# Kernel optimization log

Measured on AMD Instinct MI355X. Metric: run time of the kernel, lower is better.

## Reference

```python
import jax, jax.numpy as jnp
import numpy as np

TOP_K = 6
CAP_FACTOR = 2.0


def setup_inputs() -> dict:
    key = jax.random.key(0)
    ks = jax.random.split(key, 9)
    B, S, D, F, E, SH = 4, 2048, 512, 256, 64, 2
    return {
        "x": jax.random.normal(ks[0], (B, S, D), jnp.float32),
        "router_w": jax.random.normal(ks[1], (E, D), jnp.float32) * 0.02,
        "bias": jnp.zeros((E,), jnp.float32),
        "shared_w_gate": jax.random.normal(ks[2], (SH, F, D), jnp.float32) * 0.02,
        "shared_w_up": jax.random.normal(ks[3], (SH, F, D), jnp.float32) * 0.02,
        "shared_w_down": jax.random.normal(ks[4], (SH, D, F), jnp.float32) * 0.02,
        "w_gate": jax.random.normal(ks[5], (E, F, D), jnp.float32) * 0.02,
        "w_up": jax.random.normal(ks[6], (E, F, D), jnp.float32) * 0.02,
        "w_down": jax.random.normal(ks[7], (E, D, F), jnp.float32) * 0.02,
    }


def reference(x, router_w, bias, shared_w_gate, shared_w_up, shared_w_down, w_gate, w_up, w_down):
    B, S, D = x.shape
    E = router_w.shape[0]
    K = TOP_K
    N = B * S
    C = max(1, int(N * K * CAP_FACTOR / E))  # static per-expert capacity

    # Router logits with balancing bias (loop_idx=0 row).
    router_logits = jnp.einsum('bsd,ed->bse', x, router_w) + bias

    # Shared experts: averaged SwiGLU over SH experts, fully batched.
    hg = jnp.einsum('bsd,efd->bsef', x, shared_w_gate)
    hu = jnp.einsum('bsd,efd->bsef', x, shared_w_up)
    shared_out = jnp.einsum('bsef,edf->bsd', jax.nn.silu(hg) * hu, shared_w_down)
    shared_out = shared_out / shared_w_gate.shape[0]

    # Top-k routing, renormalised gates.
    router_probs = jax.nn.softmax(router_logits, axis=-1)
    topk_p, topk_i = jax.lax.top_k(router_probs, K)  # [B,S,K]
    topk_p = topk_p / (jnp.sum(topk_p, axis=-1, keepdims=True) + 1e-9)

    x_flat = x.reshape(N, D)
    flat_e = topk_i.reshape(-1)            # [N*K] expert ids
    flat_g = topk_p.reshape(-1)            # [N*K] gates
    token_ids = jnp.repeat(jnp.arange(N), K)

    # Stable sort by expert id -> contiguous expert groups.
    order = jnp.argsort(flat_e)            # jax argsort is stable
    se = flat_e[order]
    st = token_ids[order]
    sg = flat_g[order]

    M = se.shape[0]
    pos = jnp.arange(M)
    is_first = jnp.concatenate([jnp.ones((1,), bool), se[1:] != se[:-1]])
    group_starts = jax.lax.cummax(pos * is_first.astype(pos.dtype))
    slot = pos - group_starts              # position within expert group
    valid = slot < C                       # capacity drop
    safe_slot = jnp.where(valid, slot, C)  # overflow -> scratch slot C

    # Static-shape dispatch buffers (E, C+1, ...); slot C is scratch.
    expert_in = jnp.zeros((E, C + 1, D), x.dtype).at[se, safe_slot].set(x_flat[st])
    expert_gate = jnp.zeros((E, C + 1), x.dtype).at[se, safe_slot].set(sg)
    expert_tok = jnp.full((E, C + 1), N, jnp.int32).at[se, safe_slot].set(st.astype(jnp.int32))
    expert_mask = jnp.zeros((E, C + 1), bool).at[se, safe_slot].set(valid)

    expert_in = expert_in[:, :C]
    expert_gate = expert_gate[:, :C]
    expert_tok = expert_tok[:, :C]
    expert_mask = expert_mask[:, :C]

    # Grouped SwiGLU: three batched GEMMs over experts.
    hg = jnp.einsum('ecd,efd->ecf', expert_in, w_gate)
    hu = jnp.einsum('ecd,efd->ecf', expert_in, w_up)
    expert_out = jnp.einsum('ecf,edf->ecd', jax.nn.silu(hg) * hu, w_down)

    # Combine: scatter-add gated outputs back to tokens; row N is a sink.
    fm = expert_mask.reshape(-1)
    dst = jnp.where(fm, expert_tok.reshape(-1), N)
    fg = jnp.where(fm, expert_gate.reshape(-1), jnp.zeros((), x.dtype))
    sparse = jax.ops.segment_sum(fg[:, None] * expert_out.reshape(-1, D), dst, num_segments=N + 1)[:N]

    return shared_out + sparse.reshape(B, S, D)
```

## Files before the change

kernel.cpp:

```cpp
#include <hip/hip_runtime.h>
#include <hip/hip_bf16.h>
#include <math.h>

#define N_TOK 8192
#define D_DIM 512
#define F_DIM 256
#define E_NUM 64
#define SH_NUM 2
#define K_TOP 6
#define CAP   1536
#define M_ENT (N_TOK * K_TOP)
#define NCHUNK (M_ENT / 256)

#define EW_STRIDE 393216
#define E_TOT (E_NUM + SH_NUM)
#define X_BF_BYTES   (8388608ull)
#define WT_BYTES     ((size_t)E_TOT * EW_STRIDE * 2)
#define TOK_ROUTED   (E_NUM * CAP)
#define TOK_TOTAL    (TOK_ROUTED + SH_NUM * N_TOK)
#define EO_BYTES     ((size_t)TOK_TOTAL * D_DIM * 2)
#define RWT_BYTES    131072ull

typedef __attribute__((ext_vector_type(8))) short bf16x8;
typedef __attribute__((ext_vector_type(8))) short short8;
typedef __attribute__((ext_vector_type(4))) float f32x4;

__device__ __forceinline__ ushort f2bf(float f) {
  union { float f; unsigned u; } c; c.f = f;
  return (ushort)((c.u + 0x7FFFu + ((c.u >> 16) & 1u)) >> 16);
}
__device__ __forceinline__ float bf2f(ushort h) {
  union { unsigned u; float f; } c; c.u = ((unsigned)h) << 16;
  return c.f;
}

__global__ void router_topk(const float* __restrict__ x, const float* __restrict__ rw,
                            const float* __restrict__ bias, int* __restrict__ topk_i,
                            float* __restrict__ topk_p) {
  const int wave = threadIdx.x >> 6;
  const int lane = threadIdx.x & 63;
  const int n = blockIdx.x * 4 + wave;
  if (n >= N_TOK) return;

  const float4* xr = (const float4*)(x + (size_t)n * D_DIM);
  const float4* wr = (const float4*)(rw + (size_t)lane * D_DIM);
  float acc = 0.f;
  #pragma unroll 4
  for (int d4 = 0; d4 < D_DIM / 4; ++d4) {
    float4 xv = xr[d4]; float4 wv = wr[d4];
    acc += xv.x * wv.x + xv.y * wv.y + xv.z * wv.z + xv.w * wv.w;
  }
  float logit = acc + bias[lane];

  float m = logit;
  for (int off = 32; off > 0; off >>= 1) m = fmaxf(m, __shfl_xor(m, off));
  float p = expf(logit - m);
  float s = p;
  for (int off = 32; off > 0; off >>= 1) s += __shfl_xor(s, off);
  float prob = p / s;

  float myp = prob;
  float gsum = 0.f;
  float myg = 0.f; int myi = -1;
  for (int k = 0; k < K_TOP; ++k) {
    float bp = myp; int bi = lane;
    for (int off = 32; off > 0; off >>= 1) {
      float op = __shfl_xor(bp, off); int oi = __shfl_xor(bi, off);
      if (op > bp || (op == bp && oi < bi)) { bp = op; bi = oi; }
    }
    gsum += bp;
    if (lane == k) { myg = bp; myi = bi; }
    if (lane == bi) myp = -1.f;
  }
  if (lane < K_TOP) {
    topk_i[n * K_TOP + lane] = myi;
    topk_p[n * K_TOP + lane] = myg / (gsum + 1e-9f);
  }
}

__device__ __forceinline__ void softmax_topk_write(float logit, int n, int lane,
                                                   int* __restrict__ topk_i,
                                                   float* __restrict__ topk_p) {
  float m = logit;
  for (int off = 32; off > 0; off >>= 1) m = fmaxf(m, __shfl_xor(m, off));
  float p = expf(logit - m);
  float s = p;
  for (int off = 32; off > 0; off >>= 1) s += __shfl_xor(s, off);
  float prob = p / s;

  float myp = prob;
  float gsum = 0.f;
  float myg = 0.f; int myi = -1;
  #pragma unroll 1
  for (int k = 0; k < K_TOP; ++k) {
    float bp = myp; int bi = lane;
    for (int off = 32; off > 0; off >>= 1) {
      float op = __shfl_xor(bp, off); int oi = __shfl_xor(bi, off);
      if (op > bp || (op == bp && oi < bi)) { bp = op; bi = oi; }
    }
    gsum += bp;
    if (lane == k) { myg = bp; myi = bi; }
    if (lane == bi) myp = -1.f;
  }
  if (lane < K_TOP) {
    topk_i[n * K_TOP + lane] = myi;
    topk_p[n * K_TOP + lane] = myg / (gsum + 1e-9f);
  }
}

__global__ void __launch_bounds__(256) router_topk2(
    const float* __restrict__ x, const float* __restrict__ rwt,
    const float* __restrict__ bias, int* __restrict__ topk_i,
    float* __restrict__ topk_p) {
  const int wave = threadIdx.x >> 6;
  const int lane = threadIdx.x & 63;
  const int n0 = blockIdx.x * 32 + wave * 8;

  float acc[8];
  #pragma unroll
  for (int t = 0; t < 8; ++t) acc[t] = 0.f;

  const float4* wv4 = (const float4*)rwt;
  #pragma unroll 2
  for (int k4 = 0; k4 < 128; ++k4) {
    float4 w = wv4[k4 * 64 + lane];
    #pragma unroll
    for (int t = 0; t < 8; ++t) {
      float4 xv = *(const float4*)(x + (size_t)(n0 + t) * D_DIM + k4 * 4);
      acc[t] += xv.x * w.x + xv.y * w.y + xv.z * w.z + xv.w * w.w;
    }
  }
  float b = bias[lane];
  #pragma unroll 1
  for (int t = 0; t < 8; ++t)
    softmax_topk_write(acc[t] + b, n0 + t, lane, topk_i, topk_p);
}

__global__ void hist_kernel(const int* __restrict__ topk_i, int* __restrict__ chunk_hist) {
  __shared__ int h[E_NUM];
  const int tid = threadIdx.x;
  if (tid < E_NUM) h[tid] = 0;
  __syncthreads();
  int e = topk_i[blockIdx.x * 256 + tid];
  atomicAdd(&h[e], 1);
  __syncthreads();
  if (tid < E_NUM) chunk_hist[blockIdx.x * E_NUM + tid] = h[tid];
}

__global__ void scan_kernel(const int* __restrict__ chunk_hist, int* __restrict__ chunk_base) {
  const int e = threadIdx.x;
  int run = 0;
  for (int c = 0; c < NCHUNK; ++c) {
    chunk_base[c * E_NUM + e] = run;
    run += chunk_hist[c * E_NUM + e];
  }
}

__global__ void dispatch_kernel(const int* __restrict__ topk_i, const float* __restrict__ topk_p,
                                const int* __restrict__ chunk_base,
                                int* __restrict__ expert_tok, float* __restrict__ expert_gate,
                                int* __restrict__ entry_row) {
  __shared__ int eid[256];
  const int tid = threadIdx.x;
  const int m = blockIdx.x * 256 + tid;
  const int e = topk_i[m];
  eid[tid] = e;
  __syncthreads();
  int rank = 0;
  for (int t = 0; t < tid; ++t) rank += (eid[t] == e);
  int slot = chunk_base[blockIdx.x * E_NUM + e] + rank;
  int row = -1;
  if (slot < CAP) {
    expert_tok[e * CAP + slot] = m / K_TOP;
    expert_gate[e * CAP + slot] = topk_p[m];
    row = e * CAP + slot;
  }
  if (entry_row) entry_row[m] = row;
}


__global__ void convert_x_misc(const float* __restrict__ x, ushort* __restrict__ xb,
                               const float* __restrict__ rw, float* __restrict__ rwt,
                               int* __restrict__ tok_all, float* __restrict__ gate_all) {
  int b = blockIdx.x;
  if (b < 2048) {
    size_t idx = (size_t)b * 256 + threadIdx.x;
    const float4* s4 = (const float4*)(x + idx * 8);
    float4 v0 = s4[0], v1 = s4[1];
    short8 o;
    o[0] = f2bf(v0.x); o[1] = f2bf(v0.y); o[2] = f2bf(v0.z); o[3] = f2bf(v0.w);
    o[4] = f2bf(v1.x); o[5] = f2bf(v1.y); o[6] = f2bf(v1.z); o[7] = f2bf(v1.w);
    *(short8*)(xb + idx * 8) = o;
  } else if (b < 2080) {
    int idx = (b - 2048) * 256 + threadIdx.x;
    int e = idx >> 7, k4 = idx & 127;
    float4 v = *(const float4*)(rw + (size_t)e * D_DIM + k4 * 4);
    *(float4*)(rwt + ((size_t)k4 * 64 + e) * 4) = v;
  } else {
    int i = (b - 2080) * 256 + threadIdx.x;
    tok_all[TOK_ROUTED + i] = i & (N_TOK - 1);
    gate_all[TOK_ROUTED + i] = 0.5f;
  }
}

__global__ void convert_w(const float* __restrict__ wg_, const float* __restrict__ wu_,
                          const float* __restrict__ wd_, const float* __restrict__ swg,
                          const float* __restrict__ swu, const float* __restrict__ swd,
                          ushort* __restrict__ Wt) {
  int e = blockIdx.x / 12;
  int rem = blockIdx.x - e * 12;
  int p = rem >> 2, q = rem & 3;
  const float* src;
  if (p == 0)      src = (e < E_NUM) ? wg_ + (size_t)e * 131072 : swg + (size_t)(e - E_NUM) * 131072;
  else if (p == 1) src = (e < E_NUM) ? wu_ + (size_t)e * 131072 : swu + (size_t)(e - E_NUM) * 131072;
  else             src = (e < E_NUM) ? wd_ + (size_t)e * 131072 : swd + (size_t)(e - E_NUM) * 131072;
  ushort* dst = Wt + (size_t)e * EW_STRIDE + (size_t)p * 131072;
  #pragma unroll
  for (int i = 0; i < 16; ++i) {
    int d = q * 32768 + i * 2048 + threadIdx.x * 8;
    int ci = d >> 13;
    int r  = d & 8191;
    int nt = r >> 9;
    int rr = r & 511;
    int k8 = rr >> 7;
    int n  = nt * 16 + ((rr >> 3) & 15);
    size_t srcidx;
    if (p < 2) {
      srcidx = (size_t)n * 512 + ci * 32 + k8 * 8;
    } else {
      int np = ci >> 3, kc = ci & 7;
      srcidx = (size_t)(np * 256 + n) * 256 + kc * 32 + k8 * 8;
    }
    const float4* s4 = (const float4*)(src + srcidx);
    float4 v0 = s4[0], v1 = s4[1];
    short8 o;
    o[0] = f2bf(v0.x); o[1] = f2bf(v0.y); o[2] = f2bf(v0.z); o[3] = f2bf(v0.w);
    o[4] = f2bf(v1.x); o[5] = f2bf(v1.y); o[6] = f2bf(v1.z); o[7] = f2bf(v1.w);
    *(short8*)(dst + d) = o;
  }
}

template <bool GATHER>
__global__ void __launch_bounds__(512, 1) ffn_mfma(
    const ushort* __restrict__ xb, const ushort* __restrict__ Wt,
    const int* __restrict__ tok_all, const float* __restrict__ gate_all,
    float* __restrict__ out, ushort* __restrict__ expert_out) {
  int e, tbase;
  {
    int xcd = blockIdx.x & 7;
    int j = blockIdx.x >> 3;
    if (j < 96) {
      int ec = j / 12;
      int mt = j - ec * 12;
      e = ec * 8 + xcd;
      tbase = e * CAP + mt * 128;
      if (tok_all[tbase] < 0) return;
    } else {
      int s = xcd * 16 + (j - 96);
      int sh = s & 1, mt = s >> 1;
      e = E_NUM + sh;
      tbase = TOK_ROUTED + sh * N_TOK + mt * 128;
    }
  }
  const ushort* wbase = Wt + (size_t)e * EW_STRIDE;

  __shared__ ushort Act[32768];
  __shared__ int   toks[128];
  __shared__ float gts[128];

  const int tid = threadIdx.x;
  const int lane = tid & 63;
  const int wid = tid >> 6;
  const int wr = wid >> 2;
  const int wc = wid & 3;
  const int rl = lane & 15;
  const int hi = lane >> 4;

  if (tid < 128) {
    int t = tok_all[tbase + tid];
    toks[tid] = t;
    gts[tid] = (t >= 0) ? gate_all[tbase + tid] : 0.f;
  }
  __syncthreads();

  const ushort* xA[4];
  #pragma unroll
  for (int ri = 0; ri < 4; ++ri) {
    int t = toks[wr * 64 + ri * 16 + rl];
    xA[ri] = xb + (size_t)(t < 0 ? 0 : t) * D_DIM + hi * 8;
  }

  auto loadXr = [&](int kc, bf16x8 (&a)[4]) {
    #pragma unroll
    for (int ri = 0; ri < 4; ++ri)
      a[ri] = *(const bf16x8*)(xA[ri] + kc * 32);
  };
  auto loadW = [&](int kc, bf16x8 (&g)[4], bf16x8 (&u)[4]) {
    #pragma unroll
    for (int bi = 0; bi < 4; ++bi) {
      const ushort* p = wbase + kc * 8192 + (wc * 4 + bi) * 512 + lane * 8;
      g[bi] = *(const bf16x8*)p;
      u[bi] = *(const bf16x8*)(p + 131072);
    }
  };

  const f32x4 fzero = {0.f, 0.f, 0.f, 0.f};
  f32x4 accg[4][4], accu[4][4];
  #pragma unroll
  for (int ri = 0; ri < 4; ++ri)
    #pragma unroll
    for (int bi = 0; bi < 4; ++bi) { accg[ri][bi] = fzero; accu[ri][bi] = fzero; }

  auto guMFMA = [&](bf16x8 (&a)[4], bf16x8 (&g)[4], bf16x8 (&u)[4]) {
    __builtin_amdgcn_s_setprio(1);
    #pragma unroll
    for (int bi = 0; bi < 4; ++bi)
      #pragma unroll
      for (int ri = 0; ri < 4; ++ri) {
        accg[ri][bi] = __builtin_amdgcn_mfma_f32_16x16x32_bf16(a[ri], g[bi], accg[ri][bi], 0, 0, 0);
        accu[ri][bi] = __builtin_amdgcn_mfma_f32_16x16x32_bf16(a[ri], u[bi], accu[ri][bi], 0, 0, 0);
      }
    __builtin_amdgcn_s_setprio(0);
  };

  {
    bf16x8 gA[4], uA[4], gB[4], uB[4], aA[4], aB[4];
    loadW(0, gA, uA); loadXr(0, aA);
    #pragma unroll 1
    for (int k2 = 0; k2 < 16; k2 += 2) {
      loadW(k2 + 1, gB, uB); loadXr(k2 + 1, aB);
      guMFMA(aA, gA, uA);
      if (k2 + 2 < 16) { loadW(k2 + 2, gA, uA); loadXr(k2 + 2, aA); }
      guMFMA(aB, gB, uB);
    }
  }

  #pragma unroll
  for (int ri = 0; ri < 4; ++ri)
    #pragma unroll
    for (int bi = 0; bi < 4; ++bi) {
      int st = (wr * 4 + ri) * 8 + wc * 2 + (bi >> 1);
      int base = st * 512 + ((bi & 1) * 2 + (rl >> 3)) * 128 + (rl & 7);
      #pragma unroll
      for (int j = 0; j < 4; ++j) {
        float g = accg[ri][bi][j], u = accu[ri][bi][j];
        Act[base + (hi * 4 + j) * 8] = f2bf(g / (1.f + __expf(-g)) * u);
      }
    }

  const ushort* wdbase = wbase + 262144 + (wc >> 1) * 65536 + ((wc & 1) * 8) * 512 + lane * 8;
  auto loadWd = [&](int kc, bf16x8 (&d)[8]) {
    #pragma unroll
    for (int bj = 0; bj < 8; ++bj)
      d[bj] = *(const bf16x8*)(wdbase + kc * 8192 + bj * 512);
  };

  f32x4 accd[4][8];
  #pragma unroll
  for (int ri = 0; ri < 4; ++ri)
    #pragma unroll
    for (int bj = 0; bj < 8; ++bj) accd[ri][bj] = fzero;

  bf16x8 dA[8], dB[8];
  loadWd(0, dA);
  __syncthreads();

  auto dnMFMA = [&](int kc, bf16x8 (&d)[8]) {
    bf16x8 a[4];
    #pragma unroll
    for (int ri = 0; ri < 4; ++ri)
      a[ri] = *(const bf16x8*)(&Act[((wr * 4 + ri) * 8 + kc) * 512 + lane * 8]);
    __builtin_amdgcn_s_setprio(1);
    #pragma unroll
    for (int bj = 0; bj < 8; ++bj)
      #pragma unroll
      for (int ri = 0; ri < 4; ++ri)
        accd[ri][bj] = __builtin_amdgcn_mfma_f32_16x16x32_bf16(a[ri], d[bj], accd[ri][bj], 0, 0, 0);
    __builtin_amdgcn_s_setprio(0);
  };

  #pragma unroll 1
  for (int k2 = 0; k2 < 8; k2 += 2) {
    loadWd(k2 + 1, dB);
    dnMFMA(k2, dA);
    if (k2 + 2 < 8) loadWd(k2 + 2, dA);
    dnMFMA(k2 + 1, dB);
  }

  if (GATHER) {
    #pragma unroll
    for (int ri = 0; ri < 4; ++ri)
      #pragma unroll
      for (int j = 0; j < 4; ++j) {
        int r = wr * 64 + ri * 16 + hi * 4 + j;
        if (toks[r] < 0) continue;
        ushort* erow = expert_out + (size_t)(tbase + r) * D_DIM + wc * 128 + rl;
        #pragma unroll
        for (int bj = 0; bj < 8; ++bj)
          erow[bj * 16] = f2bf(accd[ri][bj][j]);
      }
  } else {
    #pragma unroll
    for (int ri = 0; ri < 4; ++ri)
      #pragma unroll
      for (int j = 0; j < 4; ++j) {
        int r = wr * 64 + ri * 16 + hi * 4 + j;
        int t = toks[r];
        if (t < 0) continue;
        float gt = gts[r];
        float* orow = out + (size_t)t * D_DIM + wc * 128 + rl;
        #pragma unroll
        for (int bj = 0; bj < 8; ++bj)
          atomicAdd(orow + bj * 16, gt * accd[ri][bj][j]);
      }
  }
}

__global__ void __launch_bounds__(256) gather_out(
    const ushort* __restrict__ eo, const int* __restrict__ entry_row,
    const float* __restrict__ topk_p, float* __restrict__ out) {
  const int t = blockIdx.x * 4 + (threadIdx.x >> 6);
  const int lane = threadIdx.x & 63;
  const int base = t * K_TOP;

  float acc[8];
  #pragma unroll
  for (int j = 0; j < 8; ++j) acc[j] = 0.f;

  #pragma unroll
  for (int k = 0; k < K_TOP; ++k) {
    int row = entry_row[base + k];
    if (row >= 0) {
      float g = topk_p[base + k];
      bf16x8 v = *(const bf16x8*)(eo + (size_t)row * D_DIM + lane * 8);
      #pragma unroll
      for (int j = 0; j < 8; ++j) acc[j] += g * bf2f((ushort)v[j]);
    }
  }
  #pragma unroll
  for (int sh = 0; sh < SH_NUM; ++sh) {
    int row = TOK_ROUTED + sh * N_TOK + t;
    bf16x8 v = *(const bf16x8*)(eo + (size_t)row * D_DIM + lane * 8);
    #pragma unroll
    for (int j = 0; j < 8; ++j) acc[j] += 0.5f * bf2f((ushort)v[j]);
  }
  float4* o = (float4*)(out + (size_t)t * D_DIM + lane * 8);
  o[0] = make_float4(acc[0], acc[1], acc[2], acc[3]);
  o[1] = make_float4(acc[4], acc[5], acc[6], acc[7]);
}


__global__ void __launch_bounds__(256, 2) expert_ffn_mfma(
    const float* __restrict__ x, const float* __restrict__ wg_,
    const float* __restrict__ wu_, const float* __restrict__ wd_,
    const int* __restrict__ expert_tok, const float* __restrict__ expert_gate,
    float* __restrict__ out) {
  const int e = blockIdx.x & (E_NUM - 1);
  const int mt = blockIdx.x >> 6;
  const int s0 = mt * 64;
  if (expert_tok[e * CAP + s0] < 0) return;

  __shared__ ushort Xs[64][72];
  __shared__ ushort Ws[256][72];
  __shared__ ushort Act[64][264];
  __shared__ int   toks[64];
  __shared__ float gts[64];

  const int tid = threadIdx.x;
  const int lane = tid & 63;
  const int wid = tid >> 6;
  const int rl = lane & 15;
  const int ko = (lane >> 4) * 8;
  const int rquad = (lane >> 4) * 4;

  if (tid < 64) {
    int t = expert_tok[e * CAP + s0 + tid];
    toks[tid] = t;
    gts[tid] = (t >= 0) ? expert_gate[e * CAP + s0 + tid] : 0.f;
  }
  __syncthreads();

  float4 px[4], pw[16];

  auto loadX = [&](int kb) {
    #pragma unroll
    for (int it = 0; it < 4; ++it) {
      int idx = tid + it * 256;
      int row = idx >> 4, c4 = (idx & 15) << 2;
      int t = toks[row];
      px[it] = (t >= 0) ? *(const float4*)(x + (size_t)t * D_DIM + kb * 64 + c4)
                        : make_float4(0.f, 0.f, 0.f, 0.f);
    }
  };
  auto writeX = [&]() {
    #pragma unroll
    for (int it = 0; it < 4; ++it) {
      int idx = tid + it * 256;
      int row = idx >> 4, c4 = (idx & 15) << 2;
      ushort4 h; h.x = f2bf(px[it].x); h.y = f2bf(px[it].y);
      h.z = f2bf(px[it].z); h.w = f2bf(px[it].w);
      *(ushort4*)&Xs[row][c4] = h;
    }
  };
  auto loadW = [&](const float* src, int ldk, int kb) {
    #pragma unroll
    for (int it = 0; it < 16; ++it) {
      int idx = tid + it * 256;
      int row = idx >> 4, c4 = (idx & 15) << 2;
      pw[it] = *(const float4*)(src + (size_t)row * ldk + kb * 64 + c4);
    }
  };
  auto writeW = [&]() {
    #pragma unroll
    for (int it = 0; it < 16; ++it) {
      int idx = tid + it * 256;
      int row = idx >> 4, c4 = (idx & 15) << 2;
      ushort4 h; h.x = f2bf(pw[it].x); h.y = f2bf(pw[it].y);
      h.z = f2bf(pw[it].z); h.w = f2bf(pw[it].w);
      *(ushort4*)&Ws[row][c4] = h;
    }
  };
  auto compute = [&](const ushort* Ab, int lda, f32x4 (&acc)[4][4]) {
    #pragma unroll
    for (int kk = 0; kk < 2; ++kk) {
      bf16x8 a[4], b[4];
      #pragma unroll
      for (int ri = 0; ri < 4; ++ri)
        a[ri] = *(const bf16x8*)(Ab + (size_t)(ri * 16 + rl) * lda + kk * 32 + ko);
      #pragma unroll
      for (int bi = 0; bi < 4; ++bi)
        b[bi] = *(const bf16x8*)(&Ws[wid * 64 + bi * 16 + rl][kk * 32 + ko]);
      #pragma unroll
      for (int ri = 0; ri < 4; ++ri)
        #pragma unroll
        for (int bi = 0; bi < 4; ++bi)
          acc[ri][bi] = __builtin_amdgcn_mfma_f32_16x16x32_bf16(a[ri], b[bi], acc[ri][bi], 0, 0, 0);
    }
  };

  const f32x4 fzero = {0.f, 0.f, 0.f, 0.f};

  #pragma unroll 1
  for (int which = 0; which < 2; ++which) {
    const float* wsrc = (which == 0 ? wg_ : wu_) + (size_t)e * F_DIM * D_DIM;
    f32x4 acc[4][4];
    #pragma unroll
    for (int ri = 0; ri < 4; ++ri)
      #pragma unroll
      for (int bi = 0; bi < 4; ++bi) acc[ri][bi] = fzero;

    loadX(0); loadW(wsrc, D_DIM, 0);
    writeX(); writeW();
    __syncthreads();
    for (int kb = 0; kb < 8; ++kb) {
      if (kb < 7) { loadX(kb + 1); loadW(wsrc, D_DIM, kb + 1); }
      compute(&Xs[0][0], 72, acc);
      __syncthreads();
      if (kb < 7) { writeX(); writeW(); __syncthreads(); }
    }
    #pragma unroll
    for (int ri = 0; ri < 4; ++ri)
      #pragma unroll
      for (int bi = 0; bi < 4; ++bi)
        #pragma unroll
        for (int j = 0; j < 4; ++j) {
          int r = ri * 16 + rquad + j;
          int c = wid * 64 + bi * 16 + rl;
          if (which == 0) {
            Act[r][c] = f2bf(acc[ri][bi][j]);
          } else {
            float hg = bf2f(Act[r][c]);
            float a = hg / (1.f + __expf(-hg)) * acc[ri][bi][j];
            Act[r][c] = f2bf(a);
          }
        }
    __syncthreads();
  }

  #pragma unroll 1
  for (int np = 0; np < 2; ++np) {
    const float* wsrc = wd_ + ((size_t)e * D_DIM + np * 256) * F_DIM;
    f32x4 acc[4][4];
    #pragma unroll
    for (int ri = 0; ri < 4; ++ri)
      #pragma unroll
      for (int bi = 0; bi < 4; ++bi) acc[ri][bi] = fzero;

    loadW(wsrc, F_DIM, 0); writeW();
    __syncthreads();
    for (int kb = 0; kb < 4; ++kb) {
      if (kb < 3) loadW(wsrc, F_DIM, kb + 1);
      compute(&Act[0][kb * 64], 264, acc);
      __syncthreads();
      if (kb < 3) { writeW(); __syncthreads(); }
    }
    #pragma unroll
    for (int ri = 0; ri < 4; ++ri)
      #pragma unroll
      for (int bi = 0; bi < 4; ++bi)
        #pragma unroll
        for (int j = 0; j < 4; ++j) {
          int r = ri * 16 + rquad + j;
          int t = toks[r];
          if (t >= 0) {
            int c = np * 256 + wid * 64 + bi * 16 + rl;
            atomicAdd(out + (size_t)t * D_DIM + c, gts[r] * acc[ri][bi][j]);
          }
        }
  }
}

__global__ void __launch_bounds__(256, 2) shared_ffn_mfma(
    const float* __restrict__ x, const float* __restrict__ swg,
    const float* __restrict__ swu, const float* __restrict__ swd,
    float* __restrict__ out) {
  const int row0 = blockIdx.x * 32;

  __shared__ ushort Xs[32][72];
  __shared__ ushort Ws[256][72];
  __shared__ ushort Act[32][264];

  const int tid = threadIdx.x;
  const int lane = tid & 63;
  const int wid = tid >> 6;
  const int rl = lane & 15;
  const int ko = (lane >> 4) * 8;
  const int rquad = (lane >> 4) * 4;

  float4 px[2], pw[16];

  auto loadX = [&](int kb) {
    #pragma unroll
    for (int it = 0; it < 2; ++it) {
      int idx = tid + it * 256;
      int row = idx >> 4, c4 = (idx & 15) << 2;
      px[it] = *(const float4*)(x + (size_t)(row0 + row) * D_DIM + kb * 64 + c4);
    }
  };
  auto writeX = [&]() {
    #pragma unroll
    for (int it = 0; it < 2; ++it) {
      int idx = tid + it * 256;
      int row = idx >> 4, c4 = (idx & 15) << 2;
      ushort4 h; h.x = f2bf(px[it].x); h.y = f2bf(px[it].y);
      h.z = f2bf(px[it].z); h.w = f2bf(px[it].w);
      *(ushort4*)&Xs[row][c4] = h;
    }
  };
  auto loadW = [&](const float* src, int ldk, int kb) {
    #pragma unroll
    for (int it = 0; it < 16; ++it) {
      int idx = tid + it * 256;
      int row = idx >> 4, c4 = (idx & 15) << 2;
      pw[it] = *(const float4*)(src + (size_t)row * ldk + kb * 64 + c4);
    }
  };
  auto writeW = [&]() {
    #pragma unroll
    for (int it = 0; it < 16; ++it) {
      int idx = tid + it * 256;
      int row = idx >> 4, c4 = (idx & 15) << 2;
      ushort4 h; h.x = f2bf(pw[it].x); h.y = f2bf(pw[it].y);
      h.z = f2bf(pw[it].z); h.w = f2bf(pw[it].w);
      *(ushort4*)&Ws[row][c4] = h;
    }
  };
  auto compute = [&](const ushort* Ab, int lda, f32x4 (&acc)[2][4]) {
    #pragma unroll
    for (int kk = 0; kk < 2; ++kk) {
      bf16x8 a[2], b[4];
      #pragma unroll
      for (int ri = 0; ri < 2; ++ri)
        a[ri] = *(const bf16x8*)(Ab + (size_t)(ri * 16 + rl) * lda + kk * 32 + ko);
      #pragma unroll
      for (int bi = 0; bi < 4; ++bi)
        b[bi] = *(const bf16x8*)(&Ws[wid * 64 + bi * 16 + rl][kk * 32 + ko]);
      #pragma unroll
      for (int ri = 0; ri < 2; ++ri)
        #pragma unroll
        for (int bi = 0; bi < 4; ++bi)
          acc[ri][bi] = __builtin_amdgcn_mfma_f32_16x16x32_bf16(a[ri], b[bi], acc[ri][bi], 0, 0, 0);
    }
  };

  const f32x4 fzero = {0.f, 0.f, 0.f, 0.f};
  f32x4 accd[2][2][4];
  #pragma unroll
  for (int np = 0; np < 2; ++np)
    #pragma unroll
    for (int ri = 0; ri < 2; ++ri)
      #pragma unroll
      for (int bi = 0; bi < 4; ++bi) accd[np][ri][bi] = fzero;

  #pragma unroll 1
  for (int sh = 0; sh < SH_NUM; ++sh) {
    #pragma unroll 1
    for (int which = 0; which < 2; ++which) {
      const float* wsrc = (which == 0 ? swg : swu) + (size_t)sh * F_DIM * D_DIM;
      f32x4 acc[2][4];
      #pragma unroll
      for (int ri = 0; ri < 2; ++ri)
        #pragma unroll
        for (int bi = 0; bi < 4; ++bi) acc[ri][bi] = fzero;

      loadX(0); loadW(wsrc, D_DIM, 0);
      writeX(); writeW();
      __syncthreads();
      for (int kb = 0; kb < 8; ++kb) {
        if (kb < 7) { loadX(kb + 1); loadW(wsrc, D_DIM, kb + 1); }
        compute(&Xs[0][0], 72, acc);
        __syncthreads();
        if (kb < 7) { writeX(); writeW(); __syncthreads(); }
      }
      #pragma unroll
      for (int ri = 0; ri < 2; ++ri)
        #pragma unroll
        for (int bi = 0; bi < 4; ++bi)
          #pragma unroll
          for (int j = 0; j < 4; ++j) {
            int r = ri * 16 + rquad + j;
            int c = wid * 64 + bi * 16 + rl;
            if (which == 0) {
              Act[r][c] = f2bf(acc[ri][bi][j]);
            } else {
              float hg = bf2f(Act[r][c]);
              float a = hg / (1.f + __expf(-hg)) * acc[ri][bi][j];
              Act[r][c] = f2bf(a);
            }
          }
      __syncthreads();
    }
    #pragma unroll
    for (int np = 0; np < 2; ++np) {
      const float* wsrc = swd + ((size_t)sh * D_DIM + np * 256) * F_DIM;
      loadW(wsrc, F_DIM, 0); writeW();
      __syncthreads();
      for (int kb = 0; kb < 4; ++kb) {
        if (kb < 3) loadW(wsrc, F_DIM, kb + 1);
        compute(&Act[0][kb * 64], 264, accd[np]);
        __syncthreads();
        if (kb < 3) { writeW(); __syncthreads(); }
      }
    }
  }

  #pragma unroll
  for (int np = 0; np < 2; ++np)
    #pragma unroll
    for (int ri = 0; ri < 2; ++ri)
      #pragma unroll
      for (int bi = 0; bi < 4; ++bi)
        #pragma unroll
        for (int j = 0; j < 4; ++j) {
          int r = ri * 16 + rquad + j;
          int c = np * 256 + wid * 64 + bi * 16 + rl;
          out[(size_t)(row0 + r) * D_DIM + c] = 0.5f * accd[np][ri][bi][j];
        }
}

extern "C" void kernel_launch(void* const* d_in, const int* in_sizes, int n_in,
                              void* d_out, int out_size, void* d_ws, size_t ws_size,
                              hipStream_t stream) {
  const float* x    = (const float*)d_in[0];
  const float* rw   = (const float*)d_in[1];
  const float* bias = (const float*)d_in[2];
  const float* swg  = (const float*)d_in[3];
  const float* swu  = (const float*)d_in[4];
  const float* swd  = (const float*)d_in[5];
  const float* wg   = (const float*)d_in[6];
  const float* wu   = (const float*)d_in[7];
  const float* wd   = (const float*)d_in[8];
  float* out = (float*)d_out;

  const size_t small = 2 * (size_t)M_ENT * 4 + (size_t)M_ENT * 4 +
                       2 * (size_t)NCHUNK * E_NUM * 4 + 2 * (size_t)TOK_TOTAL * 4 +
                       RWT_BYTES;
  const size_t need_mid = X_BF_BYTES + WT_BYTES + small;
  const size_t need_big = need_mid + EO_BYTES;

  if (ws_size >= need_mid) {
    const bool gather = (ws_size >= need_big);
    char* ws = (char*)d_ws;
    ushort* x_bf     = (ushort*)ws; ws += X_BF_BYTES;
    ushort* Wt       = (ushort*)ws; ws += WT_BYTES;
    int*   topk_i    = (int*)ws;    ws += (size_t)M_ENT * 4;
    float* topk_p    = (float*)ws;  ws += (size_t)M_ENT * 4;
    int*   entry_row = (int*)ws;    ws += (size_t)M_ENT * 4;
    int*   chunk_hist= (int*)ws;    ws += (size_t)NCHUNK * E_NUM * 4;
    int*   chunk_base= (int*)ws;    ws += (size_t)NCHUNK * E_NUM * 4;
    int*   tok_all   = (int*)ws;    ws += (size_t)TOK_TOTAL * 4;
    float* gate_all  = (float*)ws;  ws += (size_t)TOK_TOTAL * 4;
    float* rwt       = (float*)ws;  ws += RWT_BYTES;
    ushort* eo       = (ushort*)ws;

    convert_x_misc<<<2144, 256, 0, stream>>>(x, x_bf, rw, rwt, tok_all, gate_all);
    convert_w<<<E_TOT * 12, 256, 0, stream>>>(wg, wu, wd, swg, swu, swd, Wt);
    router_topk2<<<256, 256, 0, stream>>>(x, rwt, bias, topk_i, topk_p);
    hipMemsetAsync(tok_all, 0xFF, (size_t)TOK_ROUTED * 4, stream);
    if (!gather) hipMemsetAsync(out, 0, (size_t)out_size * 4, stream);
    hist_kernel<<<NCHUNK, 256, 0, stream>>>(topk_i, chunk_hist);
    scan_kernel<<<1, 64, 0, stream>>>(chunk_hist, chunk_base);
    dispatch_kernel<<<NCHUNK, 256, 0, stream>>>(topk_i, topk_p, chunk_base, tok_all,
                                                gate_all, entry_row);
    const int nblk = (CAP / 128) * E_NUM + 2 * (N_TOK / 128);
    if (gather) {
      ffn_mfma<true><<<nblk, 512, 0, stream>>>(x_bf, Wt, tok_all, gate_all, out, eo);
      gather_out<<<N_TOK / 4, 256, 0, stream>>>(eo, entry_row, topk_p, out);
    } else {
      ffn_mfma<false><<<nblk, 512, 0, stream>>>(x_bf, Wt, tok_all, gate_all, out, nullptr);
    }
  } else {
    char* ws = (char*)d_ws;
    int*   topk_i      = (int*)ws;   ws += (size_t)M_ENT * 4;
    float* topk_p      = (float*)ws; ws += (size_t)M_ENT * 4;
    int*   chunk_hist  = (int*)ws;   ws += (size_t)NCHUNK * E_NUM * 4;
    int*   chunk_base  = (int*)ws;   ws += (size_t)NCHUNK * E_NUM * 4;
    int*   expert_tok  = (int*)ws;   ws += (size_t)E_NUM * CAP * 4;
    float* expert_gate = (float*)ws; ws += (size_t)E_NUM * CAP * 4;

    router_topk<<<N_TOK / 4, 256, 0, stream>>>(x, rw, bias, topk_i, topk_p);
    hipMemsetAsync(expert_tok, 0xFF, (size_t)E_NUM * CAP * 4, stream);
    hist_kernel<<<NCHUNK, 256, 0, stream>>>(topk_i, chunk_hist);
    scan_kernel<<<1, 64, 0, stream>>>(chunk_hist, chunk_base);
    dispatch_kernel<<<NCHUNK, 256, 0, stream>>>(topk_i, topk_p, chunk_base, expert_tok,
                                                expert_gate, nullptr);
    shared_ffn_mfma<<<N_TOK / 32, 256, 0, stream>>>(x, swg, swu, swd, out);
    expert_ffn_mfma<<<(CAP / 64) * E_NUM, 256, 0, stream>>>(x, wg, wu, wd, expert_tok,
                                                            expert_gate, out);
  }
}
```

Baseline: 255.7 us.

## Fuse prep kernels and sum both shared experts in one FFN block

The x/router-weight conversion, weight conversion and the tok_all memset are merged into a single prep_all launch. In the FFN kernel, each shared-expert block now runs both shared experts back to back, accumulating the down projection in registers, and writes 0.5× the sum straight to out. This removes the shared-expert rows from the expert_out buffer. gather_out then adds routed contributions onto the existing out values instead of reading the shared rows. The change cuts launches, memset overhead and shared-expert output traffic, but halves the number of shared blocks while doubling their work, which may lengthen the tail.

```diff
diff --git a/kernel.cpp b/kernel.cpp
--- a/kernel.cpp
+++ b/kernel.cpp
@@ -18,7 +18,7 @@
 #define WT_BYTES     ((size_t)E_TOT * EW_STRIDE * 2)
 #define TOK_ROUTED   (E_NUM * CAP)
 #define TOK_TOTAL    (TOK_ROUTED + SH_NUM * N_TOK)
-#define EO_BYTES     ((size_t)TOK_TOTAL * D_DIM * 2)
+#define EO_BYTES     ((size_t)TOK_ROUTED * D_DIM * 2)
 #define RWT_BYTES    131072ull
 
 typedef __attribute__((ext_vector_type(8))) short bf16x8;
@@ -179,9 +179,13 @@
 }
 
 
-__global__ void convert_x_misc(const float* __restrict__ x, ushort* __restrict__ xb,
-                               const float* __restrict__ rw, float* __restrict__ rwt,
-                               int* __restrict__ tok_all, float* __restrict__ gate_all) {
+__global__ void prep_all(const float* __restrict__ x, ushort* __restrict__ xb,
+                         const float* __restrict__ rw, float* __restrict__ rwt,
+                         int* __restrict__ tok_all,
+                         const float* __restrict__ wg_, const float* __restrict__ wu_,
+                         const float* __restrict__ wd_, const float* __restrict__ swg,
+                         const float* __restrict__ swu, const float* __restrict__ swd,
+                         ushort* __restrict__ Wt) {
   int b = blockIdx.x;
   if (b < 2048) {
     size_t idx = (size_t)b * 256 + threadIdx.x;
@@ -191,24 +195,23 @@
     o[0] = f2bf(v0.x); o[1] = f2bf(v0.y); o[2] = f2bf(v0.z); o[3] = f2bf(v0.w);
     o[4] = f2bf(v1.x); o[5] = f2bf(v1.y); o[6] = f2bf(v1.z); o[7] = f2bf(v1.w);
     *(short8*)(xb + idx * 8) = o;
-  } else if (b < 2080) {
+    return;
+  }
+  if (b < 2080) {
     int idx = (b - 2048) * 256 + threadIdx.x;
     int e = idx >> 7, k4 = idx & 127;
     float4 v = *(const float4*)(rw + (size_t)e * D_DIM + k4 * 4);
     *(float4*)(rwt + ((size_t)k4 * 64 + e) * 4) = v;
-  } else {
+    return;
+  }
+  if (b < 2464) {
     int i = (b - 2080) * 256 + threadIdx.x;
-    tok_all[TOK_ROUTED + i] = i & (N_TOK - 1);
-    gate_all[TOK_ROUTED + i] = 0.5f;
-  }
-}
-
-__global__ void convert_w(const float* __restrict__ wg_, const float* __restrict__ wu_,
-                          const float* __restrict__ wd_, const float* __restrict__ swg,
-                          const float* __restrict__ swu, const float* __restrict__ swd,
-                          ushort* __restrict__ Wt) {
-  int e = blockIdx.x / 12;
-  int rem = blockIdx.x - e * 12;
+    tok_all[i] = -1;
+    return;
+  }
+  int cb = b - 2464;
+  int e = cb / 12;
+  int rem = cb - e * 12;
   int p = rem >> 2, q = rem & 3;
   const float* src;
   if (p == 0)      src = (e < E_NUM) ? wg_ + (size_t)e * 131072 : swg + (size_t)(e - E_NUM) * 131072;
@@ -245,24 +248,24 @@
     const ushort* __restrict__ xb, const ushort* __restrict__ Wt,
     const int* __restrict__ tok_all, const float* __restrict__ gate_all,
     float* __restrict__ out, ushort* __restrict__ expert_out) {
-  int e, tbase;
+  int e0, nexp, tbase, tok0;
   {
     int xcd = blockIdx.x & 7;
     int j = blockIdx.x >> 3;
     if (j < 96) {
       int ec = j / 12;
       int mt = j - ec * 12;
-      e = ec * 8 + xcd;
-      tbase = e * CAP + mt * 128;
+      e0 = ec * 8 + xcd; nexp = 1;
+      tbase = e0 * CAP + mt * 128;
       if (tok_all[tbase] < 0) return;
+      tok0 = -1;
     } else {
-      int s = xcd * 16 + (j - 96);
-      int sh = s & 1, mt = s >> 1;
-      e = E_NUM + sh;
-      tbase = TOK_ROUTED + sh * N_TOK + mt * 128;
-    }
-  }
-  const ushort* wbase = Wt + (size_t)e * EW_STRIDE;
+      int mt = xcd * 8 + (j - 96);
+      e0 = E_NUM; nexp = 2;
+      tok0 = mt * 128;
+      tbase = -1;
+    }
+  }
 
   __shared__ ushort Act[32768];
   __shared__ int   toks[128];
@@ -277,9 +280,14 @@
   const int hi = lane >> 4;
 
   if (tid < 128) {
-    int t = tok_all[tbase + tid];
-    toks[tid] = t;
-    gts[tid] = (t >= 0) ? gate_all[tbase + tid] : 0.f;
+    if (nexp == 1) {
+      int t = tok_all[tbase + tid];
+      toks[tid] = t;
+      gts[tid] = (t >= 0) ? gate_all[tbase + tid] : 0.f;
+    } else {
+      toks[tid] = tok0 + tid;
+      gts[tid] = 0.5f;
+    }
   }
   __syncthreads();
 
@@ -295,99 +303,123 @@
     for (int ri = 0; ri < 4; ++ri)
       a[ri] = *(const bf16x8*)(xA[ri] + kc * 32);
   };
-  auto loadW = [&](int kc, bf16x8 (&g)[4], bf16x8 (&u)[4]) {
-    #pragma unroll
-    for (int bi = 0; bi < 4; ++bi) {
-      const ushort* p = wbase + kc * 8192 + (wc * 4 + bi) * 512 + lane * 8;
-      g[bi] = *(const bf16x8*)p;
-      u[bi] = *(const bf16x8*)(p + 131072);
-    }
-  };
 
   const f32x4 fzero = {0.f, 0.f, 0.f, 0.f};
-  f32x4 accg[4][4], accu[4][4];
-  #pragma unroll
-  for (int ri = 0; ri < 4; ++ri)
-    #pragma unroll
-    for (int bi = 0; bi < 4; ++bi) { accg[ri][bi] = fzero; accu[ri][bi] = fzero; }
-
-  auto guMFMA = [&](bf16x8 (&a)[4], bf16x8 (&g)[4], bf16x8 (&u)[4]) {
-    __builtin_amdgcn_s_setprio(1);
-    #pragma unroll
-    for (int bi = 0; bi < 4; ++bi)
-      #pragma unroll
-      for (int ri = 0; ri < 4; ++ri) {
-        accg[ri][bi] = __builtin_amdgcn_mfma_f32_16x16x32_bf16(a[ri], g[bi], accg[ri][bi], 0, 0, 0);
-        accu[ri][bi] = __builtin_amdgcn_mfma_f32_16x16x32_bf16(a[ri], u[bi], accu[ri][bi], 0, 0, 0);
-      }
-    __builtin_amdgcn_s_setprio(0);
-  };
-
-  {
-    bf16x8 gA[4], uA[4], gB[4], uB[4], aA[4], aB[4];
-    loadW(0, gA, uA); loadXr(0, aA);
-    #pragma unroll 1
-    for (int k2 = 0; k2 < 16; k2 += 2) {
-      loadW(k2 + 1, gB, uB); loadXr(k2 + 1, aB);
-      guMFMA(aA, gA, uA);
-      if (k2 + 2 < 16) { loadW(k2 + 2, gA, uA); loadXr(k2 + 2, aA); }
-      guMFMA(aB, gB, uB);
-    }
-  }
-
-  #pragma unroll
-  for (int ri = 0; ri < 4; ++ri)
-    #pragma unroll
-    for (int bi = 0; bi < 4; ++bi) {
-      int st = (wr * 4 + ri) * 8 + wc * 2 + (bi >> 1);
-      int base = st * 512 + ((bi & 1) * 2 + (rl >> 3)) * 128 + (rl & 7);
-      #pragma unroll
-      for (int j = 0; j < 4; ++j) {
-        float g = accg[ri][bi][j], u = accu[ri][bi][j];
-        Act[base + (hi * 4 + j) * 8] = f2bf(g / (1.f + __expf(-g)) * u);
-      }
-    }
-
-  const ushort* wdbase = wbase + 262144 + (wc >> 1) * 65536 + ((wc & 1) * 8) * 512 + lane * 8;
-  auto loadWd = [&](int kc, bf16x8 (&d)[8]) {
-    #pragma unroll
-    for (int bj = 0; bj < 8; ++bj)
-      d[bj] = *(const bf16x8*)(wdbase + kc * 8192 + bj * 512);
-  };
-
   f32x4 accd[4][8];
   #pragma unroll
   for (int ri = 0; ri < 4; ++ri)
     #pragma unroll
     for (int bj = 0; bj < 8; ++bj) accd[ri][bj] = fzero;
 
-  bf16x8 dA[8], dB[8];
-  loadWd(0, dA);
-  __syncthreads();
-
-  auto dnMFMA = [&](int kc, bf16x8 (&d)[8]) {
-    bf16x8 a[4];
-    #pragma unroll
-    for (int ri = 0; ri < 4; ++ri)
-      a[ri] = *(const bf16x8*)(&Act[((wr * 4 + ri) * 8 + kc) * 512 + lane * 8]);
-    __builtin_amdgcn_s_setprio(1);
-    #pragma unroll
-    for (int bj = 0; bj < 8; ++bj)
+  #pragma unroll 1
+  for (int ei = 0; ei < nexp; ++ei) {
+    const ushort* wbase = Wt + (size_t)(e0 + ei) * EW_STRIDE;
+
+    auto loadW = [&](int kc, bf16x8 (&g)[4], bf16x8 (&u)[4]) {
+      #pragma unroll
+      for (int bi = 0; bi < 4; ++bi) {
+        const ushort* p = wbase + kc * 8192 + (wc * 4 + bi) * 512 + lane * 8;
+        g[bi] = *(const bf16x8*)p;
+        u[bi] = *(const bf16x8*)(p + 131072);
+      }
+    };
+
+    f32x4 accg[4][4], accu[4][4];
+    #pragma unroll
+    for (int ri = 0; ri < 4; ++ri)
+      #pragma unroll
+      for (int bi = 0; bi < 4; ++bi) { accg[ri][bi] = fzero; accu[ri][bi] = fzero; }
+
+    auto guMFMA = [&](bf16x8 (&a)[4], bf16x8 (&g)[4], bf16x8 (&u)[4]) {
+      __builtin_amdgcn_s_setprio(1);
+      #pragma unroll
+      for (int bi = 0; bi < 4; ++bi)
+        #pragma unroll
+        for (int ri = 0; ri < 4; ++ri) {
+          accg[ri][bi] = __builtin_amdgcn_mfma_f32_16x16x32_bf16(a[ri], g[bi], accg[ri][bi], 0, 0, 0);
+          accu[ri][bi] = __builtin_amdgcn_mfma_f32_16x16x32_bf16(a[ri], u[bi], accu[ri][bi], 0, 0, 0);
+        }
+      __builtin_amdgcn_s_setprio(0);
+    };
+
+    {
+      bf16x8 gA[4], uA[4], gB[4], uB[4], aA[4], aB[4];
+      loadW(0, gA, uA); loadXr(0, aA);
+      #pragma unroll 1
+      for (int k2 = 0; k2 < 16; k2 += 2) {
+        loadW(k2 + 1, gB, uB); loadXr(k2 + 1, aB);
+        guMFMA(aA, gA, uA);
+        if (k2 + 2 < 16) { loadW(k2 + 2, gA, uA); loadXr(k2 + 2, aA); }
+        guMFMA(aB, gB, uB);
+      }
+    }
+
+    __syncthreads();
+
+    #pragma unroll
+    for (int ri = 0; ri < 4; ++ri)
+      #pragma unroll
+      for (int bi = 0; bi < 4; ++bi) {
+        int st = (wr * 4 + ri) * 8 + wc * 2 + (bi >> 1);
+        int base = st * 512 + ((bi & 1) * 2 + (rl >> 3)) * 128 + (rl & 7);
+        #pragma unroll
+        for (int j = 0; j < 4; ++j) {
+          float g = accg[ri][bi][j], u = accu[ri][bi][j];
+          Act[base + (hi * 4 + j) * 8] = f2bf(g / (1.f + __expf(-g)) * u);
+        }
+      }
+
+    const ushort* wdbase = wbase + 262144 + (wc >> 1) * 65536 + ((wc & 1) * 8) * 512 + lane * 8;
+    auto loadWd = [&](int kc, bf16x8 (&d)[8]) {
+      #pragma unroll
+      for (int bj = 0; bj < 8; ++bj)
+        d[bj] = *(const bf16x8*)(wdbase + kc * 8192 + bj * 512);
+    };
+    auto dnMFMA = [&](int kc, bf16x8 (&d)[8]) {
+      bf16x8 a[4];
       #pragma unroll
       for (int ri = 0; ri < 4; ++ri)
-        accd[ri][bj] = __builtin_amdgcn_mfma_f32_16x16x32_bf16(a[ri], d[bj], accd[ri][bj], 0, 0, 0);
-    __builtin_amdgcn_s_setprio(0);
-  };
-
-  #pragma unroll 1
-  for (int k2 = 0; k2 < 8; k2 += 2) {
-    loadWd(k2 + 1, dB);
-    dnMFMA(k2, dA);
-    if (k2 + 2 < 8) loadWd(k2 + 2, dA);
-    dnMFMA(k2 + 1, dB);
-  }
-
-  if (GATHER) {
+        a[ri] = *(const bf16x8*)(&Act[((wr * 4 + ri) * 8 + kc) * 512 + lane * 8]);
+      __builtin_amdgcn_s_setprio(1);
+      #pragma unroll
+      for (int bj = 0; bj < 8; ++bj)
+        #pragma unroll
+        for (int ri = 0; ri < 4; ++ri)
+          accd[ri][bj] = __builtin_amdgcn_mfma_f32_16x16x32_bf16(a[ri], d[bj], accd[ri][bj], 0, 0, 0);
+      __builtin_amdgcn_s_setprio(0);
+    };
+
+    bf16x8 dA[8], dB[8];
+    loadWd(0, dA);
+    __syncthreads();
+    #pragma unroll 1
+    for (int k2 = 0; k2 < 8; k2 += 2) {
+      loadWd(k2 + 1, dB);
+      dnMFMA(k2, dA);
+      if (k2 + 2 < 8) loadWd(k2 + 2, dA);
+      dnMFMA(k2 + 1, dB);
+    }
+  }
+
+  if (nexp == 2) {
+    #pragma unroll
+    for (int ri = 0; ri < 4; ++ri)
+      #pragma unroll
+      for (int j = 0; j < 4; ++j) {
+        int r = wr * 64 + ri * 16 + hi * 4 + j;
+        int t = tok0 + r;
+        float* orow = out + (size_t)t * D_DIM + wc * 128 + rl;
+        if (GATHER) {
+          #pragma unroll
+          for (int bj = 0; bj < 8; ++bj)
+            orow[bj * 16] = 0.5f * accd[ri][bj][j];
+        } else {
+          #pragma unroll
+          for (int bj = 0; bj < 8; ++bj)
+            atomicAdd(orow + bj * 16, 0.5f * accd[ri][bj][j]);
+        }
+      }
+  } else if (GATHER) {
     #pragma unroll
     for (int ri = 0; ri < 4; ++ri)
       #pragma unroll
@@ -423,9 +455,9 @@
   const int lane = threadIdx.x & 63;
   const int base = t * K_TOP;
 
-  float acc[8];
-  #pragma unroll
-  for (int j = 0; j < 8; ++j) acc[j] = 0.f;
+  float4* o = (float4*)(out + (size_t)t * D_DIM + lane * 8);
+  float4 o0 = o[0], o1 = o[1];
+  float acc[8] = {o0.x, o0.y, o0.z, o0.w, o1.x, o1.y, o1.z, o1.w};
 
   #pragma unroll
   for (int k = 0; k < K_TOP; ++k) {
@@ -437,14 +469,6 @@
       for (int j = 0; j < 8; ++j) acc[j] += g * bf2f((ushort)v[j]);
     }
   }
-  #pragma unroll
-  for (int sh = 0; sh < SH_NUM; ++sh) {
-    int row = TOK_ROUTED + sh * N_TOK + t;
-    bf16x8 v = *(const bf16x8*)(eo + (size_t)row * D_DIM + lane * 8);
-    #pragma unroll
-    for (int j = 0; j < 8; ++j) acc[j] += 0.5f * bf2f((ushort)v[j]);
-  }
-  float4* o = (float4*)(out + (size_t)t * D_DIM + lane * 8);
   o[0] = make_float4(acc[0], acc[1], acc[2], acc[3]);
   o[1] = make_float4(acc[4], acc[5], acc[6], acc[7]);
 }
@@ -793,16 +817,15 @@
     float* rwt       = (float*)ws;  ws += RWT_BYTES;
     ushort* eo       = (ushort*)ws;
 
-    convert_x_misc<<<2144, 256, 0, stream>>>(x, x_bf, rw, rwt, tok_all, gate_all);
-    convert_w<<<E_TOT * 12, 256, 0, stream>>>(wg, wu, wd, swg, swu, swd, Wt);
+    prep_all<<<3256, 256, 0, stream>>>(x, x_bf, rw, rwt, tok_all,
+                                       wg, wu, wd, swg, swu, swd, Wt);
     router_topk2<<<256, 256, 0, stream>>>(x, rwt, bias, topk_i, topk_p);
-    hipMemsetAsync(tok_all, 0xFF, (size_t)TOK_ROUTED * 4, stream);
     if (!gather) hipMemsetAsync(out, 0, (size_t)out_size * 4, stream);
     hist_kernel<<<NCHUNK, 256, 0, stream>>>(topk_i, chunk_hist);
     scan_kernel<<<1, 64, 0, stream>>>(chunk_hist, chunk_base);
     dispatch_kernel<<<NCHUNK, 256, 0, stream>>>(topk_i, topk_p, chunk_base, tok_all,
                                                 gate_all, entry_row);
-    const int nblk = (CAP / 128) * E_NUM + 2 * (N_TOK / 128);
+    const int nblk = (CAP / 128) * E_NUM + N_TOK / 128;
     if (gather) {
       ffn_mfma<true><<<nblk, 512, 0, stream>>>(x_bf, Wt, tok_all, gate_all, out, eo);
       gather_out<<<N_TOK / 4, 256, 0, stream>>>(eo, entry_row, topk_p, out);
```

Result: slower. 378.7 us (+48.1%).

## Split gate/up and down GEMMs into passes to cut registers for occupancy

Applied to the files above, without the earlier changes.

The fused gate+up GEMM with double-buffered loads becomes two sequential passes, one for gate and one for up. The gate result is stored as bf16 in shared memory and combined with up through SiLU in the second pass. The down GEMM is likewise split into two 256-column halves with a single 16-tile accumulator, and launch bounds rise from 1 to 4 blocks per SIMD group. The goal is to free registers so more waves run at once and hide memory latency. In exchange, the x activations are loaded twice, software prefetch double-buffering is dropped, and the gate value is rounded to bf16 before the activation.

```diff
diff --git a/kernel.cpp b/kernel.cpp
--- a/kernel.cpp
+++ b/kernel.cpp
@@ -241,7 +241,7 @@
 }
 
 template <bool GATHER>
-__global__ void __launch_bounds__(512, 1) ffn_mfma(
+__global__ void __launch_bounds__(512, 4) ffn_mfma(
     const ushort* __restrict__ xb, const ushort* __restrict__ Wt,
     const int* __restrict__ tok_all, const float* __restrict__ gate_all,
     float* __restrict__ out, ushort* __restrict__ expert_out) {
@@ -283,136 +283,116 @@
   }
   __syncthreads();
 
-  const ushort* xA[4];
+  size_t xoff[4];
   #pragma unroll
   for (int ri = 0; ri < 4; ++ri) {
     int t = toks[wr * 64 + ri * 16 + rl];
-    xA[ri] = xb + (size_t)(t < 0 ? 0 : t) * D_DIM + hi * 8;
-  }
-
-  auto loadXr = [&](int kc, bf16x8 (&a)[4]) {
+    xoff[ri] = (size_t)(t < 0 ? 0 : t) * D_DIM + hi * 8;
+  }
+
+  const f32x4 fzero = {0.f, 0.f, 0.f, 0.f};
+
+  #pragma unroll 1
+  for (int which = 0; which < 2; ++which) {
+    const ushort* wsrc = wbase + which * 131072;
+    f32x4 acc[4][4];
     #pragma unroll
     for (int ri = 0; ri < 4; ++ri)
-      a[ri] = *(const bf16x8*)(xA[ri] + kc * 32);
-  };
-  auto loadW = [&](int kc, bf16x8 (&g)[4], bf16x8 (&u)[4]) {
-    #pragma unroll
-    for (int bi = 0; bi < 4; ++bi) {
-      const ushort* p = wbase + kc * 8192 + (wc * 4 + bi) * 512 + lane * 8;
-      g[bi] = *(const bf16x8*)p;
-      u[bi] = *(const bf16x8*)(p + 131072);
-    }
-  };
-
-  const f32x4 fzero = {0.f, 0.f, 0.f, 0.f};
-  f32x4 accg[4][4], accu[4][4];
-  #pragma unroll
-  for (int ri = 0; ri < 4; ++ri)
-    #pragma unroll
-    for (int bi = 0; bi < 4; ++bi) { accg[ri][bi] = fzero; accu[ri][bi] = fzero; }
-
-  auto guMFMA = [&](bf16x8 (&a)[4], bf16x8 (&g)[4], bf16x8 (&u)[4]) {
-    __builtin_amdgcn_s_setprio(1);
-    #pragma unroll
-    for (int bi = 0; bi < 4; ++bi)
-      #pragma unroll
-      for (int ri = 0; ri < 4; ++ri) {
-        accg[ri][bi] = __builtin_amdgcn_mfma_f32_16x16x32_bf16(a[ri], g[bi], accg[ri][bi], 0, 0, 0);
-        accu[ri][bi] = __builtin_amdgcn_mfma_f32_16x16x32_bf16(a[ri], u[bi], accu[ri][bi], 0, 0, 0);
+      #pragma unroll
+      for (int bi = 0; bi < 4; ++bi) acc[ri][bi] = fzero;
+
+    #pragma unroll 2
+    for (int kc = 0; kc < 16; ++kc) {
+      bf16x8 w[4], a[4];
+      #pragma unroll
+      for (int bi = 0; bi < 4; ++bi)
+        w[bi] = *(const bf16x8*)(wsrc + kc * 8192 + (wc * 4 + bi) * 512 + lane * 8);
+      #pragma unroll
+      for (int ri = 0; ri < 4; ++ri)
+        a[ri] = *(const bf16x8*)(xb + xoff[ri] + kc * 32);
+      __builtin_amdgcn_s_setprio(1);
+      #pragma unroll
+      for (int bi = 0; bi < 4; ++bi)
+        #pragma unroll
+        for (int ri = 0; ri < 4; ++ri)
+          acc[ri][bi] = __builtin_amdgcn_mfma_f32_16x16x32_bf16(a[ri], w[bi], acc[ri][bi], 0, 0, 0);
+      __builtin_amdgcn_s_setprio(0);
+    }
+
+    #pragma unroll
+    for (int ri = 0; ri < 4; ++ri)
+      #pragma unroll
+      for (int bi = 0; bi < 4; ++bi) {
+        int st = (wr * 4 + ri) * 8 + wc * 2 + (bi >> 1);
+        int base = st * 512 + ((bi & 1) * 2 + (rl >> 3)) * 128 + (rl & 7);
+        #pragma unroll
+        for (int j = 0; j < 4; ++j) {
+          int idx = base + (hi * 4 + j) * 8;
+          if (which == 0) {
+            Act[idx] = f2bf(acc[ri][bi][j]);
+          } else {
+            float hg = bf2f(Act[idx]);
+            Act[idx] = f2bf(hg / (1.f + __expf(-hg)) * acc[ri][bi][j]);
+          }
+        }
       }
-    __builtin_amdgcn_s_setprio(0);
-  };
-
-  {
-    bf16x8 gA[4], uA[4], gB[4], uB[4], aA[4], aB[4];
-    loadW(0, gA, uA); loadXr(0, aA);
-    #pragma unroll 1
-    for (int k2 = 0; k2 < 16; k2 += 2) {
-      loadW(k2 + 1, gB, uB); loadXr(k2 + 1, aB);
-      guMFMA(aA, gA, uA);
-      if (k2 + 2 < 16) { loadW(k2 + 2, gA, uA); loadXr(k2 + 2, aA); }
-      guMFMA(aB, gB, uB);
-    }
-  }
-
-  #pragma unroll
-  for (int ri = 0; ri < 4; ++ri)
-    #pragma unroll
-    for (int bi = 0; bi < 4; ++bi) {
-      int st = (wr * 4 + ri) * 8 + wc * 2 + (bi >> 1);
-      int base = st * 512 + ((bi & 1) * 2 + (rl >> 3)) * 128 + (rl & 7);
-      #pragma unroll
-      for (int j = 0; j < 4; ++j) {
-        float g = accg[ri][bi][j], u = accu[ri][bi][j];
-        Act[base + (hi * 4 + j) * 8] = f2bf(g / (1.f + __expf(-g)) * u);
-      }
-    }
-
-  const ushort* wdbase = wbase + 262144 + (wc >> 1) * 65536 + ((wc & 1) * 8) * 512 + lane * 8;
-  auto loadWd = [&](int kc, bf16x8 (&d)[8]) {
-    #pragma unroll
-    for (int bj = 0; bj < 8; ++bj)
-      d[bj] = *(const bf16x8*)(wdbase + kc * 8192 + bj * 512);
-  };
-
-  f32x4 accd[4][8];
-  #pragma unroll
-  for (int ri = 0; ri < 4; ++ri)
-    #pragma unroll
-    for (int bj = 0; bj < 8; ++bj) accd[ri][bj] = fzero;
-
-  bf16x8 dA[8], dB[8];
-  loadWd(0, dA);
+  }
   __syncthreads();
 
-  auto dnMFMA = [&](int kc, bf16x8 (&d)[8]) {
-    bf16x8 a[4];
+  #pragma unroll 1
+  for (int np = 0; np < 2; ++np) {
+    const ushort* wdsrc = wbase + 262144 + np * 65536;
+    f32x4 acc[4][4];
     #pragma unroll
     for (int ri = 0; ri < 4; ++ri)
-      a[ri] = *(const bf16x8*)(&Act[((wr * 4 + ri) * 8 + kc) * 512 + lane * 8]);
-    __builtin_amdgcn_s_setprio(1);
-    #pragma unroll
-    for (int bj = 0; bj < 8; ++bj)
+      #pragma unroll
+      for (int bi = 0; bi < 4; ++bi) acc[ri][bi] = fzero;
+
+    #pragma unroll 2
+    for (int kc = 0; kc < 8; ++kc) {
+      bf16x8 w[4], a[4];
+      #pragma unroll
+      for (int bi = 0; bi < 4; ++bi)
+        w[bi] = *(const bf16x8*)(wdsrc + kc * 8192 + (wc * 4 + bi) * 512 + lane * 8);
       #pragma unroll
       for (int ri = 0; ri < 4; ++ri)
-        accd[ri][bj] = __builtin_amdgcn_mfma_f32_16x16x32_bf16(a[ri], d[bj], accd[ri][bj], 0, 0, 0);
-    __builtin_amdgcn_s_setprio(0);
-  };
-
-  #pragma unroll 1
-  for (int k2 = 0; k2 < 8; k2 += 2) {
-    loadWd(k2 + 1, dB);
-    dnMFMA(k2, dA);
-    if (k2 + 2 < 8) loadWd(k2 + 2, dA);
-    dnMFMA(k2 + 1, dB);
-  }
-
-  if (GATHER) {
-    #pragma unroll
-    for (int ri = 0; ri < 4; ++ri)
-      #pragma unroll
-      for (int j = 0; j < 4; ++j) {
-        int r = wr * 64 + ri * 16 + hi * 4 + j;
-        if (toks[r] < 0) continue;
-        ushort* erow = expert_out + (size_t)(tbase + r) * D_DIM + wc * 128 + rl;
-        #pragma unroll
-        for (int bj = 0; bj < 8; ++bj)
-          erow[bj * 16] = f2bf(accd[ri][bj][j]);
-      }
-  } else {
-    #pragma unroll
-    for (int ri = 0; ri < 4; ++ri)
-      #pragma unroll
-      for (int j = 0; j < 4; ++j) {
-        int r = wr * 64 + ri * 16 + hi * 4 + j;
-        int t = toks[r];
-        if (t < 0) continue;
-        float gt = gts[r];
-        float* orow = out + (size_t)t * D_DIM + wc * 128 + rl;
-        #pragma unroll
-        for (int bj = 0; bj < 8; ++bj)
-          atomicAdd(orow + bj * 16, gt * accd[ri][bj][j]);
-      }
+        a[ri] = *(const bf16x8*)(&Act[((wr * 4 + ri) * 8 + kc) * 512 + lane * 8]);
+      __builtin_amdgcn_s_setprio(1);
+      #pragma unroll
+      for (int bi = 0; bi < 4; ++bi)
+        #pragma unroll
+        for (int ri = 0; ri < 4; ++ri)
+          acc[ri][bi] = __builtin_amdgcn_mfma_f32_16x16x32_bf16(a[ri], w[bi], acc[ri][bi], 0, 0, 0);
+      __builtin_amdgcn_s_setprio(0);
+    }
+
+    if (GATHER) {
+      #pragma unroll
+      for (int ri = 0; ri < 4; ++ri)
+        #pragma unroll
+        for (int j = 0; j < 4; ++j) {
+          int r = wr * 64 + ri * 16 + hi * 4 + j;
+          if (toks[r] < 0) continue;
+          ushort* erow = expert_out + (size_t)(tbase + r) * D_DIM + np * 256 + wc * 64 + rl;
+          #pragma unroll
+          for (int bi = 0; bi < 4; ++bi)
+            erow[bi * 16] = f2bf(acc[ri][bi][j]);
+        }
+    } else {
+      #pragma unroll
+      for (int ri = 0; ri < 4; ++ri)
+        #pragma unroll
+        for (int j = 0; j < 4; ++j) {
+          int r = wr * 64 + ri * 16 + hi * 4 + j;
+          int t = toks[r];
+          if (t < 0) continue;
+          float gt = gts[r];
+          float* orow = out + (size_t)t * D_DIM + np * 256 + wc * 64 + rl;
+          #pragma unroll
+          for (int bi = 0; bi < 4; ++bi)
+            atomicAdd(orow + bi * 16, gt * acc[ri][bi][j]);
+        }
+    }
   }
 }
 
```

Result: slower. 309.7 us (+21.1%).
